# Kernel tuning notes

Measured on AMD Instinct MI355X. Metric: run time of the kernel, lower is better.

Reference implementation:

```python
import jax, jax.numpy as jnp
import numpy as np

V, D, L, H, HD, FF, E, K, B, S = 32000, 768, 4, 12, 64, 2048, 8, 2, 2, 512
EPS = 1e-6
SCALE = HD ** -0.5


def rmsnorm(x, w):
    return w * x * jax.lax.rsqrt(jnp.mean(x * x, axis=-1, keepdims=True) + EPS)


def attention(x, wq, wk, wv, wo):
    # x: [B,S,D]
    q = jnp.einsum('bsd,de->bse', x, wq).reshape(B, S, H, HD)
    k = jnp.einsum('bsd,de->bse', x, wk).reshape(B, S, H, HD)
    v = jnp.einsum('bsd,de->bse', x, wv).reshape(B, S, H, HD)
    scores = jnp.einsum('bqhd,bkhd->bhqk', q, k) * SCALE
    a = jax.nn.softmax(scores, axis=-1)
    out = jnp.einsum('bhqk,bkhd->bqhd', a, v).reshape(B, S, D)
    return out @ wo


def moe(x, rw, gw, uw, dw):
    # x: [T,D]; rw: [D,E]; gw/uw: [E,D,FF]; dw: [E,FF,D]
    probs = jax.nn.softmax(x @ rw, axis=-1)            # [T,E]
    topv, topi = jax.lax.top_k(probs, K)               # [T,K]
    topv = topv / jnp.sum(topv, axis=-1, keepdims=True)
    combine = jnp.einsum('tke,tk->te', jax.nn.one_hot(topi, E, dtype=x.dtype), topv)  # [T,E]
    g = jnp.einsum('td,edf->etf', x, gw)               # [E,T,FF]
    u = jnp.einsum('td,edf->etf', x, uw)
    eo = jnp.einsum('etf,efd->etd', jax.nn.silu(g) * u, dw)  # [E,T,D]
    return jnp.einsum('etd,te->td', eo, combine)


def setup_inputs() -> dict:
    key = jax.random.key(0)
    ks = jax.random.split(key, 12)
    p = lambda k, shape: 0.02 * jax.random.normal(k, shape, jnp.float32)
    return {
        'input_ids': jax.random.randint(ks[0], (B, S), 0, V),
        'embed_tokens': p(ks[1], (V, D)),
        'embed_pos': p(ks[2], (S, D)),
        'wq': p(ks[3], (L, D, D)),
        'wk': p(ks[4], (L, D, D)),
        'wv': p(ks[5], (L, D, D)),
        'wo': p(ks[6], (L, D, D)),
        'norm1_w': jnp.ones((L, D), jnp.float32),
        'norm2_w': jnp.ones((L, D), jnp.float32),
        'router_w': p(ks[7], (L, D, E)),
        'gate_w': p(ks[8], (L, E, D, FF)),
        'up_w': p(ks[9], (L, E, D, FF)),
        'down_w': p(ks[10], (L, E, FF, D)),
        'final_norm_w': jnp.ones((D,), jnp.float32),
        'lm_head_w': p(ks[11], (D, V)),
    }


def reference(input_ids, embed_tokens, embed_pos, wq, wk, wv, wo, norm1_w, norm2_w,
              router_w, gate_w, up_w, down_w, final_norm_w, lm_head_w):
    x = embed_tokens[input_ids] + embed_pos[None, :, :]   # [B,S,D]
    for l in range(L):
        x = x + attention(rmsnorm(x, norm1_w[l]), wq[l], wk[l], wv[l], wo[l])
        t = rmsnorm(x, norm2_w[l]).reshape(-1, D)
        x = x + moe(t, router_w[l], gate_w[l], up_w[l], down_w[l]).reshape(B, S, D)
    logits = rmsnorm(x, final_norm_w) @ lm_head_w        # [B,S,V]
    return logits
```

## Files before the change

### kernel.cpp

```cpp
#include <hip/hip_runtime.h>
#include <math.h>

#define TT   1024
#define DM   768
#define NH   12
#define HD   64
#define FFD  2048
#define NE   8
#define SQ   512
#define NB   2
#define NL   4
#define NV   32000
#define REPS 1e-6f
#define QB   16

typedef float f32x4 __attribute__((ext_vector_type(4)));
typedef short s16x8 __attribute__((ext_vector_type(8)));

__device__ __forceinline__ float b2f(ushort u) {
  return __uint_as_float(((unsigned)u) << 16);
}
__device__ __forceinline__ ushort f2b(float f) {
  unsigned i = __float_as_uint(f);
  return (ushort)((i + 0x7FFFu + ((i >> 16) & 1u)) >> 16);
}

__global__ __launch_bounds__(256) void k_embed(const int* __restrict__ ids,
    const float* __restrict__ tok, const float* __restrict__ pos, float* __restrict__ x) {
  int t = blockIdx.x; int s = t % SQ; int id = ids[t];
  for (int d = threadIdx.x; d < DM; d += 256)
    x[t * DM + d] = tok[(size_t)id * DM + d] + pos[s * DM + d];
}

__global__ __launch_bounds__(64) void k_router(const float* __restrict__ xn,
    const float* __restrict__ rw, int* __restrict__ topi, float* __restrict__ topw,
    int* __restrict__ posb, int* __restrict__ slot, int* __restrict__ counts) {
  int t = blockIdx.x, l = threadIdx.x;
  float acc[NE] = {};
  for (int d = l; d < DM; d += 64) {
    float xv = xn[t * DM + d];
    const float* r = &rw[d * NE];
#pragma unroll
    for (int e = 0; e < NE; ++e) acc[e] += xv * r[e];
  }
#pragma unroll
  for (int off = 32; off > 0; off >>= 1)
#pragma unroll
    for (int e = 0; e < NE; ++e) acc[e] += __shfl_down(acc[e], off, 64);
  if (l == 0) {
    float mx = acc[0];
#pragma unroll
    for (int e = 1; e < NE; ++e) mx = fmaxf(mx, acc[e]);
    float p[NE], sum = 0.f;
#pragma unroll
    for (int e = 0; e < NE; ++e) { p[e] = expf(acc[e] - mx); sum += p[e]; }
#pragma unroll
    for (int e = 0; e < NE; ++e) p[e] /= sum;
    int i0 = 0;
    for (int e = 1; e < NE; ++e) if (p[e] > p[i0]) i0 = e;
    int i1 = (i0 == 0) ? 1 : 0;
    for (int e = 0; e < NE; ++e) if (e != i0 && p[e] > p[i1]) i1 = e;
    float w0 = p[i0], w1 = p[i1], inv = 1.f / (w0 + w1);
    w0 *= inv; w1 *= inv;
    int p0 = atomicAdd(&counts[i0], 1);
    int p1 = atomicAdd(&counts[i1], 1);
    topi[2 * t] = i0; topi[2 * t + 1] = i1;
    topw[2 * t] = w0; topw[2 * t + 1] = w1;
    posb[2 * t] = p0; posb[2 * t + 1] = p1;
    slot[i0 * TT + p0] = t; slot[i1 * TT + p1] = t;
  }
}

__global__ __launch_bounds__(256) void k_combine(const float* __restrict__ eo,
    const int* __restrict__ topi, const float* __restrict__ topw,
    const int* __restrict__ posb, const int* __restrict__ counts, float* __restrict__ x) {
  int t = blockIdx.x;
  int pre[NE]; int a = 0;
#pragma unroll
  for (int e = 0; e < NE; ++e) { pre[e] = a; a += counts[e]; }
  int r0 = pre[topi[2 * t]] + posb[2 * t];
  int r1 = pre[topi[2 * t + 1]] + posb[2 * t + 1];
  float w0 = topw[2 * t], w1 = topw[2 * t + 1];
  for (int d = threadIdx.x; d < DM; d += 256)
    x[t * DM + d] += w0 * eo[(size_t)r0 * DM + d] + w1 * eo[(size_t)r1 * DM + d];
}

__global__ __launch_bounds__(256) void k_attn2(const float* __restrict__ qkv,
    ushort* __restrict__ aoh, ushort* __restrict__ aol) {
  __shared__ float Qs[QB][64];
  __shared__ float KVs[128][68];
  __shared__ float sc[QB][516];
  __shared__ float red[256];
  __shared__ float mrow[QB], invr[QB];
  int qt = blockIdx.x, h = blockIdx.y, b = blockIdx.z;
  int tid = threadIdx.x;
  int q0 = qt * QB;
  const float* base = qkv + (size_t)(b * SQ) * (3 * DM);
  {
    int qi = tid >> 4, d4 = (tid & 15) * 4;
    *(float4*)&Qs[qi][d4] = *(const float4*)&base[(size_t)(q0 + qi) * (3 * DM) + h * HD + d4];
  }
  for (int kt = 0; kt < 4; ++kt) {
    __syncthreads();
    {
      int kk = tid >> 4, d4 = (tid & 15) * 4;
#pragma unroll
      for (int i = 0; i < 8; ++i)
        *(float4*)&KVs[kk + 16 * i][d4] =
            *(const float4*)&base[(size_t)(kt * 128 + kk + 16 * i) * (3 * DM) + DM + h * HD + d4];
    }
    __syncthreads();
    int q2 = tid >> 5, k4 = tid & 31;
    float a0[4] = {}, a1[4] = {};
#pragma unroll
    for (int i = 0; i < 16; ++i) {
      float4 qa = *(float4*)&Qs[2 * q2][4 * i];
      float4 qb = *(float4*)&Qs[2 * q2 + 1][4 * i];
#pragma unroll
      for (int j = 0; j < 4; ++j) {
        float4 kv = *(float4*)&KVs[k4 + 32 * j][4 * i];
        a0[j] += qa.x * kv.x + qa.y * kv.y + qa.z * kv.z + qa.w * kv.w;
        a1[j] += qb.x * kv.x + qb.y * kv.y + qb.z * kv.z + qb.w * kv.w;
      }
    }
#pragma unroll
    for (int j = 0; j < 4; ++j) {
      sc[2 * q2][kt * 128 + 32 * j + k4] = a0[j] * 0.125f;
      sc[2 * q2 + 1][kt * 128 + 32 * j + k4] = a1[j] * 0.125f;
    }
  }
  __syncthreads();
  int row = tid & 15, seg = tid >> 4;
  float m = -1e30f;
  for (int i = 0; i < 32; ++i) m = fmaxf(m, sc[row][seg + 16 * i]);
  red[tid] = m; __syncthreads();
  if (tid < QB) {
    float mm = red[tid];
#pragma unroll
    for (int j = 1; j < 16; ++j) mm = fmaxf(mm, red[tid + 16 * j]);
    mrow[tid] = mm;
  }
  __syncthreads();
  m = mrow[row];
  float s = 0.f;
  for (int i = 0; i < 32; ++i) {
    int c = seg + 16 * i;
    float e = expf(sc[row][c] - m);
    sc[row][c] = e; s += e;
  }
  red[tid] = s; __syncthreads();
  if (tid < QB) {
    float ss = red[tid];
#pragma unroll
    for (int j = 1; j < 16; ++j) ss += red[tid + 16 * j];
    invr[tid] = 1.0f / ss;
  }
  float4 o = {0.f, 0.f, 0.f, 0.f};
  int q = tid >> 4, d4 = (tid & 15) * 4;
  for (int vt = 0; vt < 4; ++vt) {
    __syncthreads();
    {
      int kk = tid >> 4, dd = (tid & 15) * 4;
#pragma unroll
      for (int i = 0; i < 8; ++i)
        *(float4*)&KVs[kk + 16 * i][dd] =
            *(const float4*)&base[(size_t)(vt * 128 + kk + 16 * i) * (3 * DM) + 2 * DM + h * HD + dd];
    }
    __syncthreads();
    for (int kk = 0; kk < 128; ++kk) {
      float w = sc[q][vt * 128 + kk];
      float4 v = *(float4*)&KVs[kk][d4];
      o.x += w * v.x; o.y += w * v.y; o.z += w * v.z; o.w += w * v.w;
    }
  }
  float iv = invr[q];
  size_t ob = (size_t)(b * SQ + q0 + q) * DM + h * HD + d4;
  float ov[4] = {o.x * iv, o.y * iv, o.z * iv, o.w * iv};
#pragma unroll
  for (int j = 0; j < 4; ++j) {
    ushort hh = f2b(ov[j]);
    aoh[ob + j] = hh;
    aol[ob + j] = f2b(ov[j] - b2f(hh));
  }
}

__global__ __launch_bounds__(256) void k_rmsnorm_sb(const float* __restrict__ x,
    const float* __restrict__ w, float* __restrict__ y,
    ushort* __restrict__ yh, ushort* __restrict__ yl, int* __restrict__ zc) {
  __shared__ float red[256];
  int t = blockIdx.x, tid = threadIdx.x;
  if (zc && t == 0 && tid < NE) zc[tid] = 0;
  float ss = 0.f;
  for (int d = tid; d < DM; d += 256) { float v = x[t * DM + d]; ss += v * v; }
  red[tid] = ss; __syncthreads();
  for (int s = 128; s > 0; s >>= 1) { if (tid < s) red[tid] += red[tid + s]; __syncthreads(); }
  float inv = 1.0f / sqrtf(red[0] / (float)DM + REPS);
  for (int d = tid; d < DM; d += 256) {
    float v = w[d] * x[t * DM + d] * inv;
    ushort h = f2b(v);
    y[t * DM + d] = v;
    yh[t * DM + d] = h;
    yl[t * DM + d] = f2b(v - b2f(h));
  }
}

__global__ __launch_bounds__(256) void k_rmsnorm_b(const float* __restrict__ x,
    const float* __restrict__ w, ushort* __restrict__ y) {
  __shared__ float red[256];
  int t = blockIdx.x, tid = threadIdx.x;
  float ss = 0.f;
  for (int d = tid; d < DM; d += 256) { float v = x[t * DM + d]; ss += v * v; }
  red[tid] = ss; __syncthreads();
  for (int s = 128; s > 0; s >>= 1) { if (tid < s) red[tid] += red[tid + s]; __syncthreads(); }
  float inv = 1.0f / sqrtf(red[0] / (float)DM + REPS);
  for (int d = tid; d < DM; d += 256)
    y[t * DM + d] = f2b(w[d] * x[t * DM + d] * inv);
}

#define EPI_RES  1
#define EPI_F32  2
#define EPI_GU   3
#define EPI_DOWN 4
#define MODE_B   0
#define MODE_QKV 1
#define MODE_GU  2

template<int BM, int BN, int MODE, int EPI, int RM, int NBX, int PREC, int DEC>
__global__ __launch_bounds__(256) void k_gmm2(
    const ushort* __restrict__ Ah, const ushort* __restrict__ Al,
    const float* __restrict__ B0, const float* __restrict__ B1, const float* __restrict__ B2,
    long long bstride, ushort* __restrict__ Ch, ushort* __restrict__ Cl,
    float* __restrict__ Cf,
    int M, int K, int ldb, int ldc,
    const int* __restrict__ slot, const int* __restrict__ counts) {
  constexpr int NEg  = (RM == 0) ? 1 : NE;
  constexpr int P    = NBX * NEg;
  constexpr int Ppad = ((P + 7) / 8) * 8;
  constexpr int MB   = TT / BM;
  int id = blockIdx.x;
  int m, pp;
  if (DEC == 0) { m = id / Ppad; pp = id % Ppad; }
  else {
    int xcd = id & 7, j = id >> 3;
    m = j % MB;
    pp = (j / MB) * 8 + xcd;
  }
  if (pp >= P) return;
  int e = pp / NBX;
  int x = pp % NBX;

  int cnt = (RM == 0) ? M : counts[e];
  int m0 = m * BM;
  if (m0 >= cnt) return;
  int n0 = x * BN;
  int off = 0;
  if (RM != 0) {
#pragma unroll
    for (int i = 0; i < NE; ++i) if (i < e) off += counts[i];
  }

  constexpr int WM = (BM == 128) ? 64 : ((BN == 128) ? 64 : 32);
  constexpr int WN = (BM == 128) ? 64 : 32;
  constexpr int MI = WM / 16, NI = WN / 16;

  __shared__ __align__(16) ushort Ahs[BM * 40];
  __shared__ __align__(16) ushort Als[(PREC == 2) ? BM * 40 : 16];
  __shared__ __align__(16) ushort Bhs[BN * 40];
  __shared__ __align__(16) ushort Bls[(PREC == 2) ? BN * 40 : 16];

  int tid = threadIdx.x;
  int wave = tid >> 6, lane = tid & 63;
  int wr, wc;
  if (BM == 128)      { wr = wave >> 1; wc = wave & 1; }
  else if (BN == 128) { wr = 0;         wc = wave;     }
  else                { wr = wave >> 1; wc = wave & 1; }
  int moff;
  if (BM == 64 && BN == 128) moff = 0; else moff = wr * ((BM == 128) ? 64 : 32);
  int noff = wc * WN;

  int arA = tid >> 2, kcA = tid & 3;
  int ar1 = tid >> 2, ar2 = ar1 + 64;
  size_t aoff1 = 0, aoff2 = 0;
  if (BM == 64) {
    int rowi;
    if (RM == 0)      rowi = m0 + arA;
    else if (RM == 1) rowi = slot[e * TT + min(m0 + arA, cnt - 1)];
    else              rowi = off + min(m0 + arA, cnt - 1);
    aoff1 = (size_t)rowi * K;
  } else {
    if (RM == 0) {
      aoff1 = (size_t)(m0 + ar1) * K;
      aoff2 = (size_t)(m0 + ar2) * K;
    } else if (RM == 1) {
      aoff1 = (size_t)slot[e * TT + min(m0 + ar1, cnt - 1)] * K;
      aoff2 = (size_t)slot[e * TT + min(m0 + ar2, cnt - 1)] * K;
    } else {
      aoff1 = (size_t)(off + min(m0 + ar1, cnt - 1)) * K;
      aoff2 = (size_t)(off + min(m0 + ar2, cnt - 1)) * K;
    }
  }

  int rB = tid & 63, ko = tid >> 6;
  auto bcol = [&](int r) -> const float* {
    if (MODE == MODE_QKV) {
      int mat = x / (NBX / 3);
      const float* Bm = (mat == 0) ? B0 : ((mat == 1) ? B1 : B2);
      return Bm + (x % (NBX / 3)) * BN + r;
    } else if (MODE == MODE_GU) {
      const float* Bg = B0 + (size_t)e * bstride;
      const float* Bu = B1 + (size_t)e * bstride;
      return ((((r) >> 4) & 1) ? Bu : Bg) + x * (BN / 2) + ((((r) >> 5) << 4) | ((r) & 15));
    }
    return B0 + (size_t)e * bstride + n0 + r;
  };
  const float* bs0 = bcol(rB);
  const float* bs1 = (BN == 128) ? bcol(rB + 64) : nullptr;

  s16x8 rah1, rah2, ral1, ral2;
  float vb0[8], vb1[8];

  auto loadA = [&](int kk) {
    if (BM == 64) {
      rah1 = *(const s16x8*)(Ah + aoff1 + kk + kcA * 8);
      if (PREC == 2) ral1 = *(const s16x8*)(Al + aoff1 + kk + kcA * 8);
    } else {
      rah1 = *(const s16x8*)(Ah + aoff1 + kk + kcA * 8);
      rah2 = *(const s16x8*)(Ah + aoff2 + kk + kcA * 8);
      if (PREC == 2) {
        ral1 = *(const s16x8*)(Al + aoff1 + kk + kcA * 8);
        ral2 = *(const s16x8*)(Al + aoff2 + kk + kcA * 8);
      }
    }
  };
  auto loadB = [&](int kk) {
#pragma unroll
    for (int i = 0; i < 8; ++i)
      vb0[i] = bs0[(size_t)(kk + ko * 8 + i) * ldb];
    if (BN == 128) {
#pragma unroll
      for (int i = 0; i < 8; ++i)
        vb1[i] = bs1[(size_t)(kk + ko * 8 + i) * ldb];
    }
  };
  auto storeLDS = [&]() {
    if (BM == 64) {
      *(s16x8*)&Ahs[arA * 40 + kcA * 8] = rah1;
      if (PREC == 2) *(s16x8*)&Als[arA * 40 + kcA * 8] = ral1;
    } else {
      *(s16x8*)&Ahs[ar1 * 40 + kcA * 8] = rah1;
      *(s16x8*)&Ahs[ar2 * 40 + kcA * 8] = rah2;
      if (PREC == 2) {
        *(s16x8*)&Als[ar1 * 40 + kcA * 8] = ral1;
        *(s16x8*)&Als[ar2 * 40 + kcA * 8] = ral2;
      }
    }
    s16x8 h0, l0;
#pragma unroll
    for (int i = 0; i < 8; ++i) {
      ushort h = f2b(vb0[i]);
      h0[i] = (short)h;
      if (PREC == 2) l0[i] = (short)f2b(vb0[i] - b2f(h));
    }
    *(s16x8*)&Bhs[rB * 40 + ko * 8] = h0;
    if (PREC == 2) *(s16x8*)&Bls[rB * 40 + ko * 8] = l0;
    if (BN == 128) {
      s16x8 h1, l1;
#pragma unroll
      for (int i = 0; i < 8; ++i) {
        ushort h = f2b(vb1[i]);
        h1[i] = (short)h;
        if (PREC == 2) l1[i] = (short)f2b(vb1[i] - b2f(h));
      }
      *(s16x8*)&Bhs[(rB + 64) * 40 + ko * 8] = h1;
      if (PREC == 2) *(s16x8*)&Bls[(rB + 64) * 40 + ko * 8] = l1;
    }
  };

  f32x4 zr = {0.f, 0.f, 0.f, 0.f};
  f32x4 acc[MI][NI];
#pragma unroll
  for (int i = 0; i < MI; ++i)
#pragma unroll
    for (int j = 0; j < NI; ++j) acc[i][j] = zr;

  int rl = lane & 15, g = lane >> 4;
  loadA(0); loadB(0);
  for (int k0 = 0; k0 < K; k0 += 32) {
    __syncthreads();
    storeLDS();
    __syncthreads();
    if (k0 + 32 < K) { loadA(k0 + 32); loadB(k0 + 32); }
#pragma unroll
    for (int mi = 0; mi < MI; ++mi) {
      int ra = (moff + mi * 16 + rl) * 40 + g * 8;
      s16x8 avh = *(const s16x8*)&Ahs[ra];
      s16x8 avl;
      if (PREC == 2) avl = *(const s16x8*)&Als[ra];
#pragma unroll
      for (int ni = 0; ni < NI; ++ni) {
        int rb = (noff + ni * 16 + rl) * 40 + g * 8;
        s16x8 bvh = *(const s16x8*)&Bhs[rb];
        f32x4 a = acc[mi][ni];
        if (PREC == 2) {
          s16x8 bvl = *(const s16x8*)&Bls[rb];
          a = __builtin_amdgcn_mfma_f32_16x16x32_bf16(avl, bvh, a, 0, 0, 0);
          a = __builtin_amdgcn_mfma_f32_16x16x32_bf16(avh, bvl, a, 0, 0, 0);
        }
        a = __builtin_amdgcn_mfma_f32_16x16x32_bf16(avh, bvh, a, 0, 0, 0);
        acc[mi][ni] = a;
      }
    }
  }

  int rg4 = (lane >> 4) * 4;
#pragma unroll
  for (int mi = 0; mi < MI; ++mi) {
#pragma unroll
    for (int rg = 0; rg < 4; ++rg) {
      int rloc = m0 + moff + mi * 16 + rg4 + rg;
      if ((EPI == EPI_GU || EPI == EPI_DOWN) && rloc >= cnt) continue;
      if (EPI == EPI_GU) {
        float gv = acc[mi][0][rg], uv = acc[mi][1][rg];
        float hv = gv / (1.f + __expf(-gv)) * uv;
        int fq = (n0 + noff) >> 5;
        size_t ix = (size_t)(off + rloc) * ldc + fq * 16 + rl;
        ushort h = f2b(hv);
        Ch[ix] = h;
        if (PREC == 2) Cl[ix] = f2b(hv - b2f(h));
      } else if (EPI == EPI_RES) {
#pragma unroll
        for (int ni = 0; ni < NI; ++ni) {
          size_t ix = (size_t)rloc * ldc + n0 + noff + ni * 16 + rl;
          Cf[ix] += acc[mi][ni][rg];
        }
      } else if (EPI == EPI_F32) {
#pragma unroll
        for (int ni = 0; ni < NI; ++ni)
          Cf[(size_t)rloc * ldc + n0 + noff + ni * 16 + rl] = acc[mi][ni][rg];
      } else {
#pragma unroll
        for (int ni = 0; ni < NI; ++ni)
          Cf[(size_t)(off + rloc) * ldc + n0 + noff + ni * 16 + rl] = acc[mi][ni][rg];
      }
    }
  }
}

extern "C" void kernel_launch(void* const* d_in, const int* in_sizes, int n_in,
                              void* d_out, int out_size, void* d_ws, size_t ws_size,
                              hipStream_t stream) {
  (void)in_sizes; (void)n_in; (void)out_size; (void)ws_size;
  const int*   ids = (const int*)d_in[0];
  const float* tok = (const float*)d_in[1];
  const float* pos = (const float*)d_in[2];
  const float* wq  = (const float*)d_in[3];
  const float* wk  = (const float*)d_in[4];
  const float* wv  = (const float*)d_in[5];
  const float* wo  = (const float*)d_in[6];
  const float* n1w = (const float*)d_in[7];
  const float* n2w = (const float*)d_in[8];
  const float* rw  = (const float*)d_in[9];
  const float* gw  = (const float*)d_in[10];
  const float* uw  = (const float*)d_in[11];
  const float* dw  = (const float*)d_in[12];
  const float* fnw = (const float*)d_in[13];
  const float* lmw = (const float*)d_in[14];
  float* out = (float*)d_out;

  char* p = (char*)d_ws;
  auto alloc = [&](size_t bytes) { char* r = p; p += (bytes + 255) & ~(size_t)255; return r; };
  float*  x    = (float*)alloc((size_t)TT * DM * 4);
  float*  xn   = (float*)alloc((size_t)TT * DM * 4);
  ushort* xh   = (ushort*)alloc((size_t)TT * DM * 2);
  ushort* xl   = (ushort*)alloc((size_t)TT * DM * 2);
  float*  qkv  = (float*)alloc((size_t)TT * 3 * DM * 4);
  ushort* aoh  = (ushort*)alloc((size_t)TT * DM * 2);
  ushort* aol  = (ushort*)alloc((size_t)TT * DM * 2);
  ushort* Hh   = (ushort*)alloc((size_t)2 * TT * FFD * 2);
  ushort* Hl   = (ushort*)alloc((size_t)2 * TT * FFD * 2);
  float*  eo   = (float*)alloc((size_t)2 * TT * DM * 4);
  float*  topw = (float*)alloc((size_t)2 * TT * 4);
  int* topi    = (int*)alloc((size_t)2 * TT * 4);
  int* posb    = (int*)alloc((size_t)2 * TT * 4);
  int* slot    = (int*)alloc((size_t)NE * TT * 4);
  int* counts  = (int*)alloc(256);
  ushort* xnb  = (ushort*)alloc((size_t)TT * DM * 2);

  k_embed<<<TT, 256, 0, stream>>>(ids, tok, pos, x);
  for (int l = 0; l < NL; ++l) {
    k_rmsnorm_sb<<<TT, 256, 0, stream>>>(x, n1w + l * DM, xn, xh, xl, nullptr);
    k_gmm2<64, 64, MODE_QKV, EPI_F32, 0, 36, 2, 0><<<16 * 40, 256, 0, stream>>>(
        xh, xl, wq + (size_t)l * DM * DM, wk + (size_t)l * DM * DM, wv + (size_t)l * DM * DM,
        0, nullptr, nullptr, qkv, TT, DM, DM, 3 * DM, nullptr, nullptr);
    k_attn2<<<dim3(SQ / QB, NH, NB), 256, 0, stream>>>(qkv, aoh, aol);
    k_gmm2<64, 64, MODE_B, EPI_RES, 0, 12, 2, 0><<<16 * 16, 256, 0, stream>>>(
        aoh, aol, wo + (size_t)l * DM * DM, nullptr, nullptr,
        0, nullptr, nullptr, x, TT, DM, DM, DM, nullptr, nullptr);

    k_rmsnorm_sb<<<TT, 256, 0, stream>>>(x, n2w + l * DM, xn, xh, xl, counts);
    k_router<<<TT, 64, 0, stream>>>(xn, rw + (size_t)l * DM * NE, topi, topw, posb, slot, counts);
    if (l < NL - 1) {
      k_gmm2<64, 128, MODE_GU, EPI_GU, 1, 32, 2, 0><<<16 * 256, 256, 0, stream>>>(
          xh, xl, gw + (size_t)l * NE * DM * FFD, uw + (size_t)l * NE * DM * FFD, nullptr,
          (long long)DM * FFD, Hh, Hl, nullptr, TT, DM, FFD, FFD, slot, counts);
      k_gmm2<64, 64, MODE_B, EPI_DOWN, 2, 12, 2, 0><<<16 * 96, 256, 0, stream>>>(
          Hh, Hl, dw + (size_t)l * NE * FFD * DM, nullptr, nullptr,
          (long long)FFD * DM, nullptr, nullptr, eo, TT, FFD, DM, DM, nullptr, counts);
    } else {
      k_gmm2<64, 128, MODE_GU, EPI_GU, 1, 32, 1, 0><<<16 * 256, 256, 0, stream>>>(
          xh, nullptr, gw + (size_t)l * NE * DM * FFD, uw + (size_t)l * NE * DM * FFD, nullptr,
          (long long)DM * FFD, Hh, nullptr, nullptr, TT, DM, FFD, FFD, slot, counts);
      k_gmm2<64, 64, MODE_B, EPI_DOWN, 2, 12, 1, 0><<<16 * 96, 256, 0, stream>>>(
          Hh, nullptr, dw + (size_t)l * NE * FFD * DM, nullptr, nullptr,
          (long long)FFD * DM, nullptr, nullptr, eo, TT, FFD, DM, DM, nullptr, counts);
    }
    k_combine<<<TT, 256, 0, stream>>>(eo, topi, topw, posb, counts, x);
  }

  k_rmsnorm_b<<<TT, 256, 0, stream>>>(x, fnw, xnb);
  k_gmm2<64, 128, MODE_B, EPI_F32, 0, 250, 1, 2><<<16 * 256, 256, 0, stream>>>(
      xnb, nullptr, lmw, nullptr, nullptr,
      0, nullptr, nullptr, out, TT, DM, NV, NV, nullptr, nullptr);
}
```

Before: 1.434 ms.

## Fuse router into rmsnorm, combine into next rmsnorm, truncate weight bf16 conversion

Merges the second RMSNorm with the router matmul and top-2 selection, and merges the MoE combine with the next layer's RMSNorm (or the final norm). This removes several kernel launches per layer and the fp32 normalized-activation round trip. Expert counters for all layers are now zeroed once in the embed kernel, and top-2 weights come straight from the logit difference, skipping the full softmax. Weight and hidden-activation bf16 splits switch from round-to-nearest to truncation, which is cheaper but slightly less accurate.

```diff
diff --git a/kernel.cpp b/kernel.cpp
--- a/kernel.cpp
+++ b/kernel.cpp
@@ -24,44 +24,86 @@
   unsigned i = __float_as_uint(f);
   return (ushort)((i + 0x7FFFu + ((i >> 16) & 1u)) >> 16);
 }
+__device__ __forceinline__ ushort t2b(float f) {
+  return (ushort)(__float_as_uint(f) >> 16);
+}
 
 __global__ __launch_bounds__(256) void k_embed(const int* __restrict__ ids,
-    const float* __restrict__ tok, const float* __restrict__ pos, float* __restrict__ x) {
-  int t = blockIdx.x; int s = t % SQ; int id = ids[t];
+    const float* __restrict__ tok, const float* __restrict__ pos, float* __restrict__ x,
+    int* __restrict__ counts4) {
+  int t = blockIdx.x;
+  if (t == 0 && threadIdx.x < NL * NE) counts4[threadIdx.x] = 0;
+  int s = t % SQ; int id = ids[t];
   for (int d = threadIdx.x; d < DM; d += 256)
     x[t * DM + d] = tok[(size_t)id * DM + d] + pos[s * DM + d];
 }
 
-__global__ __launch_bounds__(64) void k_router(const float* __restrict__ xn,
-    const float* __restrict__ rw, int* __restrict__ topi, float* __restrict__ topw,
+__global__ __launch_bounds__(256) void k_rmsnorm_sb(const float* __restrict__ x,
+    const float* __restrict__ w, ushort* __restrict__ yh, ushort* __restrict__ yl) {
+  __shared__ float red[256];
+  int t = blockIdx.x, tid = threadIdx.x;
+  float ss = 0.f;
+  for (int d = tid; d < DM; d += 256) { float v = x[t * DM + d]; ss += v * v; }
+  red[tid] = ss; __syncthreads();
+  for (int s = 128; s > 0; s >>= 1) { if (tid < s) red[tid] += red[tid + s]; __syncthreads(); }
+  float inv = 1.0f / sqrtf(red[0] / (float)DM + REPS);
+  for (int d = tid; d < DM; d += 256) {
+    float v = w[d] * x[t * DM + d] * inv;
+    ushort h = f2b(v);
+    yh[t * DM + d] = h;
+    yl[t * DM + d] = f2b(v - b2f(h));
+  }
+}
+
+__global__ __launch_bounds__(256) void k_rmsnorm_rt(const float* __restrict__ x,
+    const float* __restrict__ nw, const float* __restrict__ rw,
+    ushort* __restrict__ yh, ushort* __restrict__ yl,
+    int* __restrict__ topi, float* __restrict__ topw,
     int* __restrict__ posb, int* __restrict__ slot, int* __restrict__ counts) {
-  int t = blockIdx.x, l = threadIdx.x;
+  __shared__ float red[256];
+  __shared__ float rw4[4][NE];
+  int t = blockIdx.x, tid = threadIdx.x;
+  float xs[3];
+  float ss = 0.f;
+#pragma unroll
+  for (int i = 0; i < 3; ++i) {
+    float v = x[t * DM + tid + 256 * i];
+    xs[i] = v; ss += v * v;
+  }
+  red[tid] = ss; __syncthreads();
+  for (int s = 128; s > 0; s >>= 1) { if (tid < s) red[tid] += red[tid + s]; __syncthreads(); }
+  float inv = 1.0f / sqrtf(red[0] / (float)DM + REPS);
   float acc[NE] = {};
-  for (int d = l; d < DM; d += 64) {
-    float xv = xn[t * DM + d];
+#pragma unroll
+  for (int i = 0; i < 3; ++i) {
+    int d = tid + 256 * i;
+    float v = nw[d] * xs[i] * inv;
+    ushort h = f2b(v);
+    yh[t * DM + d] = h;
+    yl[t * DM + d] = f2b(v - b2f(h));
     const float* r = &rw[d * NE];
 #pragma unroll
-    for (int e = 0; e < NE; ++e) acc[e] += xv * r[e];
+    for (int e = 0; e < NE; ++e) acc[e] += v * r[e];
   }
 #pragma unroll
   for (int off = 32; off > 0; off >>= 1)
 #pragma unroll
     for (int e = 0; e < NE; ++e) acc[e] += __shfl_down(acc[e], off, 64);
-  if (l == 0) {
-    float mx = acc[0];
-#pragma unroll
-    for (int e = 1; e < NE; ++e) mx = fmaxf(mx, acc[e]);
-    float p[NE], sum = 0.f;
-#pragma unroll
-    for (int e = 0; e < NE; ++e) { p[e] = expf(acc[e] - mx); sum += p[e]; }
-#pragma unroll
-    for (int e = 0; e < NE; ++e) p[e] /= sum;
+  int wv = tid >> 6, ln = tid & 63;
+  if (ln == 0)
+#pragma unroll
+    for (int e = 0; e < NE; ++e) rw4[wv][e] = acc[e];
+  __syncthreads();
+  if (tid == 0) {
+    float lg[NE];
+#pragma unroll
+    for (int e = 0; e < NE; ++e) lg[e] = rw4[0][e] + rw4[1][e] + rw4[2][e] + rw4[3][e];
     int i0 = 0;
-    for (int e = 1; e < NE; ++e) if (p[e] > p[i0]) i0 = e;
+    for (int e = 1; e < NE; ++e) if (lg[e] > lg[i0]) i0 = e;
     int i1 = (i0 == 0) ? 1 : 0;
-    for (int e = 0; e < NE; ++e) if (e != i0 && p[e] > p[i1]) i1 = e;
-    float w0 = p[i0], w1 = p[i1], inv = 1.f / (w0 + w1);
-    w0 *= inv; w1 *= inv;
+    for (int e = 0; e < NE; ++e) if (e != i0 && lg[e] > lg[i1]) i1 = e;
+    float e1 = __expf(lg[i1] - lg[i0]);
+    float w0 = 1.f / (1.f + e1), w1 = e1 / (1.f + e1);
     int p0 = atomicAdd(&counts[i0], 1);
     int p1 = atomicAdd(&counts[i1], 1);
     topi[2 * t] = i0; topi[2 * t + 1] = i1;
@@ -71,18 +113,44 @@
   }
 }
 
-__global__ __launch_bounds__(256) void k_combine(const float* __restrict__ eo,
+template<int FINAL>
+__global__ __launch_bounds__(256) void k_combine_norm(const float* __restrict__ eo,
     const int* __restrict__ topi, const float* __restrict__ topw,
-    const int* __restrict__ posb, const int* __restrict__ counts, float* __restrict__ x) {
-  int t = blockIdx.x;
+    const int* __restrict__ posb, const int* __restrict__ counts,
+    float* __restrict__ x, const float* __restrict__ w,
+    ushort* __restrict__ yh, ushort* __restrict__ yl) {
+  __shared__ float red[256];
+  int t = blockIdx.x, tid = threadIdx.x;
   int pre[NE]; int a = 0;
 #pragma unroll
   for (int e = 0; e < NE; ++e) { pre[e] = a; a += counts[e]; }
   int r0 = pre[topi[2 * t]] + posb[2 * t];
   int r1 = pre[topi[2 * t + 1]] + posb[2 * t + 1];
   float w0 = topw[2 * t], w1 = topw[2 * t + 1];
-  for (int d = threadIdx.x; d < DM; d += 256)
-    x[t * DM + d] += w0 * eo[(size_t)r0 * DM + d] + w1 * eo[(size_t)r1 * DM + d];
+  float nv[3];
+  float ss = 0.f;
+#pragma unroll
+  for (int i = 0; i < 3; ++i) {
+    int d = tid + 256 * i;
+    float v = x[t * DM + d] + w0 * eo[(size_t)r0 * DM + d] + w1 * eo[(size_t)r1 * DM + d];
+    x[t * DM + d] = v;
+    nv[i] = v; ss += v * v;
+  }
+  red[tid] = ss; __syncthreads();
+  for (int s = 128; s > 0; s >>= 1) { if (tid < s) red[tid] += red[tid + s]; __syncthreads(); }
+  float inv = 1.0f / sqrtf(red[0] / (float)DM + REPS);
+#pragma unroll
+  for (int i = 0; i < 3; ++i) {
+    int d = tid + 256 * i;
+    float u = w[d] * nv[i] * inv;
+    if (FINAL) {
+      yh[t * DM + d] = f2b(u);
+    } else {
+      ushort h = f2b(u);
+      yh[t * DM + d] = h;
+      yl[t * DM + d] = f2b(u - b2f(h));
+    }
+  }
 }
 
 __global__ __launch_bounds__(256) void k_attn2(const float* __restrict__ qkv,
@@ -182,39 +250,6 @@
     aoh[ob + j] = hh;
     aol[ob + j] = f2b(ov[j] - b2f(hh));
   }
-}
-
-__global__ __launch_bounds__(256) void k_rmsnorm_sb(const float* __restrict__ x,
-    const float* __restrict__ w, float* __restrict__ y,
-    ushort* __restrict__ yh, ushort* __restrict__ yl, int* __restrict__ zc) {
-  __shared__ float red[256];
-  int t = blockIdx.x, tid = threadIdx.x;
-  if (zc && t == 0 && tid < NE) zc[tid] = 0;
-  float ss = 0.f;
-  for (int d = tid; d < DM; d += 256) { float v = x[t * DM + d]; ss += v * v; }
-  red[tid] = ss; __syncthreads();
-  for (int s = 128; s > 0; s >>= 1) { if (tid < s) red[tid] += red[tid + s]; __syncthreads(); }
-  float inv = 1.0f / sqrtf(red[0] / (float)DM + REPS);
-  for (int d = tid; d < DM; d += 256) {
-    float v = w[d] * x[t * DM + d] * inv;
-    ushort h = f2b(v);
-    y[t * DM + d] = v;
-    yh[t * DM + d] = h;
-    yl[t * DM + d] = f2b(v - b2f(h));
-  }
-}
-
-__global__ __launch_bounds__(256) void k_rmsnorm_b(const float* __restrict__ x,
-    const float* __restrict__ w, ushort* __restrict__ y) {
-  __shared__ float red[256];
-  int t = blockIdx.x, tid = threadIdx.x;
-  float ss = 0.f;
-  for (int d = tid; d < DM; d += 256) { float v = x[t * DM + d]; ss += v * v; }
-  red[tid] = ss; __syncthreads();
-  for (int s = 128; s > 0; s >>= 1) { if (tid < s) red[tid] += red[tid + s]; __syncthreads(); }
-  float inv = 1.0f / sqrtf(red[0] / (float)DM + REPS);
-  for (int d = tid; d < DM; d += 256)
-    y[t * DM + d] = f2b(w[d] * x[t * DM + d] * inv);
 }
 
 #define EPI_RES  1
@@ -357,9 +392,9 @@
     s16x8 h0, l0;
 #pragma unroll
     for (int i = 0; i < 8; ++i) {
-      ushort h = f2b(vb0[i]);
+      ushort h = t2b(vb0[i]);
       h0[i] = (short)h;
-      if (PREC == 2) l0[i] = (short)f2b(vb0[i] - b2f(h));
+      if (PREC == 2) l0[i] = (short)t2b(vb0[i] - b2f(h));
     }
     *(s16x8*)&Bhs[rB * 40 + ko * 8] = h0;
     if (PREC == 2) *(s16x8*)&Bls[rB * 40 + ko * 8] = l0;
@@ -367,9 +402,9 @@
       s16x8 h1, l1;
 #pragma unroll
       for (int i = 0; i < 8; ++i) {
-        ushort h = f2b(vb1[i]);
+        ushort h = t2b(vb1[i]);
         h1[i] = (short)h;
-        if (PREC == 2) l1[i] = (short)f2b(vb1[i] - b2f(h));
+        if (PREC == 2) l1[i] = (short)t2b(vb1[i] - b2f(h));
       }
       *(s16x8*)&Bhs[(rB + 64) * 40 + ko * 8] = h1;
       if (PREC == 2) *(s16x8*)&Bls[(rB + 64) * 40 + ko * 8] = l1;
@@ -424,9 +459,9 @@
         float hv = gv / (1.f + __expf(-gv)) * uv;
         int fq = (n0 + noff) >> 5;
         size_t ix = (size_t)(off + rloc) * ldc + fq * 16 + rl;
-        ushort h = f2b(hv);
+        ushort h = t2b(hv);
         Ch[ix] = h;
-        if (PREC == 2) Cl[ix] = f2b(hv - b2f(h));
+        if (PREC == 2) Cl[ix] = t2b(hv - b2f(h));
       } else if (EPI == EPI_RES) {
 #pragma unroll
         for (int ni = 0; ni < NI; ++ni) {
@@ -470,7 +505,6 @@
   char* p = (char*)d_ws;
   auto alloc = [&](size_t bytes) { char* r = p; p += (bytes + 255) & ~(size_t)255; return r; };
   float*  x    = (float*)alloc((size_t)TT * DM * 4);
-  float*  xn   = (float*)alloc((size_t)TT * DM * 4);
   ushort* xh   = (ushort*)alloc((size_t)TT * DM * 2);
   ushort* xl   = (ushort*)alloc((size_t)TT * DM * 2);
   float*  qkv  = (float*)alloc((size_t)TT * 3 * DM * 4);
@@ -483,12 +517,13 @@
   int* topi    = (int*)alloc((size_t)2 * TT * 4);
   int* posb    = (int*)alloc((size_t)2 * TT * 4);
   int* slot    = (int*)alloc((size_t)NE * TT * 4);
-  int* counts  = (int*)alloc(256);
+  int* counts4 = (int*)alloc(256);
   ushort* xnb  = (ushort*)alloc((size_t)TT * DM * 2);
 
-  k_embed<<<TT, 256, 0, stream>>>(ids, tok, pos, x);
+  k_embed<<<TT, 256, 0, stream>>>(ids, tok, pos, x, counts4);
+  k_rmsnorm_sb<<<TT, 256, 0, stream>>>(x, n1w, xh, xl);
   for (int l = 0; l < NL; ++l) {
-    k_rmsnorm_sb<<<TT, 256, 0, stream>>>(x, n1w + l * DM, xn, xh, xl, nullptr);
+    int* counts = counts4 + NE * l;
     k_gmm2<64, 64, MODE_QKV, EPI_F32, 0, 36, 2, 0><<<16 * 40, 256, 0, stream>>>(
         xh, xl, wq + (size_t)l * DM * DM, wk + (size_t)l * DM * DM, wv + (size_t)l * DM * DM,
         0, nullptr, nullptr, qkv, TT, DM, DM, 3 * DM, nullptr, nullptr);
@@ -497,8 +532,8 @@
         aoh, aol, wo + (size_t)l * DM * DM, nullptr, nullptr,
         0, nullptr, nullptr, x, TT, DM, DM, DM, nullptr, nullptr);
 
-    k_rmsnorm_sb<<<TT, 256, 0, stream>>>(x, n2w + l * DM, xn, xh, xl, counts);
-    k_router<<<TT, 64, 0, stream>>>(xn, rw + (size_t)l * DM * NE, topi, topw, posb, slot, counts);
+    k_rmsnorm_rt<<<TT, 256, 0, stream>>>(x, n2w + l * DM, rw + (size_t)l * DM * NE,
+                                         xh, xl, topi, topw, posb, slot, counts);
     if (l < NL - 1) {
       k_gmm2<64, 128, MODE_GU, EPI_GU, 1, 32, 2, 0><<<16 * 256, 256, 0, stream>>>(
           xh, xl, gw + (size_t)l * NE * DM * FFD, uw + (size_t)l * NE * DM * FFD, nullptr,
@@ -506,6 +541,8 @@
       k_gmm2<64, 64, MODE_B, EPI_DOWN, 2, 12, 2, 0><<<16 * 96, 256, 0, stream>>>(
           Hh, Hl, dw + (size_t)l * NE * FFD * DM, nullptr, nullptr,
           (long long)FFD * DM, nullptr, nullptr, eo, TT, FFD, DM, DM, nullptr, counts);
+      k_combine_norm<0><<<TT, 256, 0, stream>>>(eo, topi, topw, posb, counts,
+                                                x, n1w + (size_t)(l + 1) * DM, xh, xl);
     } else {
       k_gmm2<64, 128, MODE_GU, EPI_GU, 1, 32, 1, 0><<<16 * 256, 256, 0, stream>>>(
           xh, nullptr, gw + (size_t)l * NE * DM * FFD, uw + (size_t)l * NE * DM * FFD, nullptr,
@@ -513,11 +550,11 @@
       k_gmm2<64, 64, MODE_B, EPI_DOWN, 2, 12, 1, 0><<<16 * 96, 256, 0, stream>>>(
           Hh, nullptr, dw + (size_t)l * NE * FFD * DM, nullptr, nullptr,
           (long long)FFD * DM, nullptr, nullptr, eo, TT, FFD, DM, DM, nullptr, counts);
-    }
-    k_combine<<<TT, 256, 0, stream>>>(eo, topi, topw, posb, counts, x);
-  }
-
-  k_rmsnorm_b<<<TT, 256, 0, stream>>>(x, fnw, xnb);
+      k_combine_norm<1><<<TT, 256, 0, stream>>>(eo, topi, topw, posb, counts,
+                                                x, fnw, xnb, nullptr);
+    }
+  }
+
   k_gmm2<64, 128, MODE_B, EPI_F32, 0, 250, 1, 2><<<16 * 256, 256, 0, stream>>>(
       xnb, nullptr, lmw, nullptr, nullptr,
       0, nullptr, nullptr, out, TT, DM, NV, NV, nullptr, nullptr);
```

Measured after the change: 1.338 ms (median of 4 runs). 6.7% less time.
